# Kernel optimization log

Hardware: AMD Instinct MI355X
Metric: run time of the kernel (lower is better)

The kernel has to match this reference:

```python
import jax, jax.numpy as jnp
import numpy as np

B, S, H = 2, 2048, 4096
NH = 32
HD = H // NH  # 128


def setup_inputs() -> dict:
    key = jax.random.key(0)
    ks = jax.random.split(key, 8)
    scale = 0.02
    hidden_states = jax.random.normal(ks[0], (B, S, H), jnp.float32)
    residual = jax.random.normal(ks[1], (B, S, H), jnp.float32)
    # ALiBi bias per (batch*head) over kv positions, broadcast over q dim
    alibi = jax.random.normal(ks[2], (B * NH, 1, S), jnp.float32) * 0.1
    # causal mask: True where attention is disallowed (j > i)
    causal = jnp.triu(jnp.ones((S, S), dtype=bool), k=1)
    attention_mask = jnp.broadcast_to(causal[None, None], (B, 1, S, S))
    W_qkv = jax.random.normal(ks[3], (3 * H, H), jnp.float32) * scale
    b_qkv = jax.random.normal(ks[4], (3 * H,), jnp.float32) * scale
    W_dense = jax.random.normal(ks[5], (H, H), jnp.float32) * scale
    b_dense = jax.random.normal(ks[6], (H,), jnp.float32) * scale
    return {
        "hidden_states": hidden_states,
        "residual": residual,
        "alibi": alibi,
        "attention_mask": attention_mask,
        "W_qkv": W_qkv,
        "b_qkv": b_qkv,
        "W_dense": W_dense,
        "b_dense": b_dense,
    }


def reference(hidden_states, residual, alibi, attention_mask, W_qkv, b_qkv, W_dense, b_dense):
    b, s, h = hidden_states.shape
    inv_norm = 1.0 / np.sqrt(HD).astype(np.float32)
    # fused QKV projection: [B,S,3H]
    fused = jnp.einsum("bsh,oh->bso", hidden_states, W_qkv) + b_qkv
    fused = fused.reshape(b, s, NH, 3, HD)
    q, k, v = fused[..., 0, :], fused[..., 1, :], fused[..., 2, :]  # [B,S,NH,HD]
    # scores = alibi + inv_norm * Q K^T   (baddbmm with beta=1, alpha=inv_norm)
    scores = jnp.einsum("bqhd,bkhd->bhqk", q, k) * inv_norm
    scores = scores + alibi.reshape(b, NH, 1, s)
    attn_weights = jnp.where(attention_mask, jnp.float32(-100000.0), scores)
    probs = jax.nn.softmax(attn_weights.astype(jnp.float32), axis=-1).astype(scores.dtype)
    # context: [B,S,NH,HD] -> merge heads -> [B,S,H]
    ctx = jnp.einsum("bhqk,bkhd->bqhd", probs, v).reshape(b, s, h)
    out = jnp.einsum("bsh,oh->bso", ctx, W_dense) + b_dense
    return residual + out
```

## Files before the change

### kernel.cpp

```cpp
#include <hip/hip_runtime.h>

#define B_ 2
#define S_ 2048
#define H_ 4096
#define NH_ 32
#define HD_ 128
#define LOG2E 1.44269504088896340736f

typedef unsigned short u16;
typedef __bf16 bf16x8 __attribute__((ext_vector_type(8)));
typedef float floatx4 __attribute__((ext_vector_type(4)));

__device__ __forceinline__ u16 f2bf(float f) {
  union { float f; unsigned u; } v;
  v.f = f;
  unsigned r = v.u + 0x7FFFu + ((v.u >> 16) & 1u);
  return (u16)(r >> 16);
}

__device__ __forceinline__ void dma16(const u16* g, u16* l) {
  __builtin_amdgcn_global_load_lds(
      (const __attribute__((address_space(1))) void*)g,
      (__attribute__((address_space(3))) void*)l, 16, 0, 0);
}

__global__ __launch_bounds__(256) void cast_f32_bf16(const float* __restrict__ in,
                                                     u16* __restrict__ out, int n4) {
  int i = blockIdx.x * 256 + threadIdx.x;
  if (i >= n4) return;
  float4 f = reinterpret_cast<const float4*>(in)[i];
  ushort4 o;
  o.x = f2bf(f.x); o.y = f2bf(f.y); o.z = f2bf(f.z); o.w = f2bf(f.w);
  reinterpret_cast<ushort4*>(out)[i] = o;
}

template<int EPI>
__global__ __launch_bounds__(256) void gemm_bt(
    const u16* __restrict__ A, const u16* __restrict__ Bm, int K,
    const float* __restrict__ bias, const float* __restrict__ resid,
    float* __restrict__ outf,
    u16* __restrict__ qo, u16* __restrict__ ko, u16* __restrict__ vto) {
  __shared__ __align__(16) u16 sA[128 * 32];
  __shared__ __align__(16) u16 sB[128 * 32];
  const int tid  = threadIdx.x;
  const int wave = tid >> 6, lane = tid & 63;
  const int lrow = lane & 15, quad = lane >> 4;
  const int wm = (wave >> 1) * 64, wn = (wave & 1) * 64;
  const int m0 = blockIdx.y * 128, n0 = blockIdx.x * 128;

  const u16* gA[2]; const u16* gB[2];
#pragma unroll
  for (int jj = 0; jj < 2; ++jj) {
    int L  = wave * 16 + jj * 8 + (lane >> 3);
    int sp = (lane & 7) ^ (L & 7);
    int row = 2 * L + (sp >> 2), kc = (sp & 3) * 8;
    gA[jj] = A + (size_t)(m0 + row) * K + kc;
    gB[jj] = Bm + (size_t)(n0 + row) * K + kc;
  }

  const int ssw  = (((lrow & 1) << 2) | quad) ^ ((lrow >> 1) & 7);
  const int aoff = ((wm + lrow) >> 1) * 64 + ssw * 8;
  const int boff = ((wn + lrow) >> 1) * 64 + ssw * 8;

  const floatx4 zf = {0.f, 0.f, 0.f, 0.f};
  floatx4 acc[4][4];
#pragma unroll
  for (int i = 0; i < 4; ++i)
#pragma unroll
    for (int j = 0; j < 4; ++j) acc[i][j] = zf;

  for (int k0 = 0; k0 < K; k0 += 32) {
    __syncthreads();
#pragma unroll
    for (int jj = 0; jj < 2; ++jj) {
      dma16(gA[jj], &sA[(wave * 2 + jj) * 512]);
      dma16(gB[jj], &sB[(wave * 2 + jj) * 512]);
      gA[jj] += 32; gB[jj] += 32;
    }
    __syncthreads();

    bf16x8 af[4], bf[4];
#pragma unroll
    for (int mi = 0; mi < 4; ++mi) af[mi] = *(const bf16x8*)&sA[aoff + mi * 512];
#pragma unroll
    for (int ni = 0; ni < 4; ++ni) bf[ni] = *(const bf16x8*)&sB[boff + ni * 512];
#pragma unroll
    for (int mi = 0; mi < 4; ++mi)
#pragma unroll
      for (int ni = 0; ni < 4; ++ni)
        acc[mi][ni] = __builtin_amdgcn_mfma_f32_16x16x32_bf16(af[mi], bf[ni], acc[mi][ni], 0, 0, 0);
  }

#pragma unroll
  for (int mi = 0; mi < 4; ++mi)
#pragma unroll
    for (int ni = 0; ni < 4; ++ni)
#pragma unroll
      for (int r = 0; r < 4; ++r) {
        int m = m0 + wm + mi * 16 + quad * 4 + r;
        int n = n0 + wn + ni * 16 + lrow;
        float v = acc[mi][ni][r] + bias[n];
        if (EPI == 0) {
          int b = m >> 11, s = m & (S_ - 1);
          int nh = n / (3 * HD_);
          int rem = n - nh * 3 * HD_;
          int which = rem >> 7, d = rem & (HD_ - 1);
          int bh = b * NH_ + nh;
          if (which == 0)      qo[(bh * S_ + s) * HD_ + d] = f2bf(v * 0.08838834764831845f);
          else if (which == 1) ko[(bh * S_ + s) * HD_ + d] = f2bf(v);
          else                 vto[(bh * HD_ + d) * S_ + s] = f2bf(v);
        } else {
          int idx = m * H_ + n;
          outf[idx] = v + resid[idx];
        }
      }
}

#define SKSTR 136
#define SVSTR 72
#define SPSTR 72

__global__ __launch_bounds__(256) void attn_kernel(
    const u16* __restrict__ Qb, const u16* __restrict__ Kb,
    const u16* __restrict__ Vt, const float* __restrict__ alibi,
    u16* __restrict__ ctx) {
  __shared__ __align__(16) u16 sK[64 * SKSTR];
  __shared__ __align__(16) u16 sV[128 * SVSTR];
  __shared__ __align__(16) u16 sP[4 * 16 * SPSTR];
  const int tid  = threadIdx.x;
  const int wave = tid >> 6, lane = tid & 63;
  const int lrow = lane & 15, quad = lane >> 4;
  const int qt = blockIdx.x, bh = blockIdx.y;
  const int qbase = qt * 64;
  const int qrow0 = qbase + wave * 16 + quad * 4;

  const floatx4 zf = {0.f, 0.f, 0.f, 0.f};

  bf16x8 aq[4];
  {
    const u16* qptr = Qb + (bh * S_ + qbase + wave * 16 + lrow) * HD_;
#pragma unroll
    for (int kc = 0; kc < 4; ++kc) aq[kc] = *(const bf16x8*)(qptr + kc * 32 + quad * 8);
  }

  floatx4 o[8];
#pragma unroll
  for (int di = 0; di < 8; ++di) o[di] = zf;
  float m_r[4] = {-1e30f, -1e30f, -1e30f, -1e30f};
  float l_r[4] = {0.f, 0.f, 0.f, 0.f};
  u16* sp = &sP[wave * 16 * SPSTR];

  for (int t = 0; t <= qt; ++t) {
    const int kv0 = t * 64;
    __syncthreads();
#pragma unroll
    for (int rr = 0; rr < 4; ++rr) {
      int flat = rr * 256 + tid;
      {
        int row = flat >> 4, c = flat & 15;
        *(uint4*)&sK[row * SKSTR + c * 8] =
            *(const uint4*)&Kb[(bh * S_ + kv0 + row) * HD_ + c * 8];
      }
      {
        int row = flat >> 3, c = flat & 7;
        *(uint4*)&sV[row * SVSTR + c * 8] =
            *(const uint4*)&Vt[(bh * HD_ + row) * S_ + kv0 + c * 8];
      }
    }
    __syncthreads();

    floatx4 sc[4];
#pragma unroll
    for (int ni = 0; ni < 4; ++ni) {
      floatx4 a = zf;
#pragma unroll
      for (int kc = 0; kc < 4; ++kc) {
        bf16x8 bfrag = *(const bf16x8*)&sK[(ni * 16 + lrow) * SKSTR + kc * 32 + quad * 8];
        a = __builtin_amdgcn_mfma_f32_16x16x32_bf16(aq[kc], bfrag, a, 0, 0, 0);
      }
      sc[ni] = a;
    }

    float al[4];
#pragma unroll
    for (int ni = 0; ni < 4; ++ni) al[ni] = alibi[bh * S_ + kv0 + ni * 16 + lrow];
    const bool diag = (t == qt);

    float p[4][4], alpha[4];
#pragma unroll
    for (int r = 0; r < 4; ++r) {
      float mx = -1e30f;
#pragma unroll
      for (int ni = 0; ni < 4; ++ni) {
        float scv = sc[ni][r] + al[ni];
        if (diag && (kv0 + ni * 16 + lrow) > (qrow0 + r)) scv = -1e30f;
        p[ni][r] = scv;
        mx = fmaxf(mx, scv);
      }
#pragma unroll
      for (int off = 1; off < 16; off <<= 1) mx = fmaxf(mx, __shfl_xor(mx, off));
      float mn = fmaxf(m_r[r], mx);
      float a_ = exp2f((m_r[r] - mn) * LOG2E);
      float s_ = 0.f;
#pragma unroll
      for (int ni = 0; ni < 4; ++ni) {
        float pv = exp2f((p[ni][r] - mn) * LOG2E);
        p[ni][r] = pv;
        s_ += pv;
      }
#pragma unroll
      for (int off = 1; off < 16; off <<= 1) s_ += __shfl_xor(s_, off);
      l_r[r] = l_r[r] * a_ + s_;
      m_r[r] = mn;
      alpha[r] = a_;
    }
#pragma unroll
    for (int di = 0; di < 8; ++di)
#pragma unroll
      for (int r = 0; r < 4; ++r) o[di][r] *= alpha[r];

#pragma unroll
    for (int ni = 0; ni < 4; ++ni)
#pragma unroll
      for (int r = 0; r < 4; ++r)
        sp[(quad * 4 + r) * SPSTR + ni * 16 + lrow] = f2bf(p[ni][r]);
    __syncthreads();

#pragma unroll
    for (int kc = 0; kc < 2; ++kc) {
      bf16x8 afrag = *(const bf16x8*)&sp[lrow * SPSTR + kc * 32 + quad * 8];
#pragma unroll
      for (int di = 0; di < 8; ++di) {
        bf16x8 bfrag = *(const bf16x8*)&sV[(di * 16 + lrow) * SVSTR + kc * 32 + quad * 8];
        o[di] = __builtin_amdgcn_mfma_f32_16x16x32_bf16(afrag, bfrag, o[di], 0, 0, 0);
      }
    }
  }

  const int b = bh >> 5, nh = bh & (NH_ - 1);
#pragma unroll
  for (int di = 0; di < 8; ++di)
#pragma unroll
    for (int r = 0; r < 4; ++r) {
      int q = qrow0 + r;
      float v = o[di][r] / l_r[r];
      ctx[(b * S_ + q) * H_ + nh * HD_ + di * 16 + lrow] = f2bf(v);
    }
}

extern "C" void kernel_launch(void* const* d_in, const int* in_sizes, int n_in,
                              void* d_out, int out_size, void* d_ws, size_t ws_size,
                              hipStream_t stream) {
  const float* hs    = (const float*)d_in[0];
  const float* resid = (const float*)d_in[1];
  const float* alibi = (const float*)d_in[2];
  const float* Wqkv  = (const float*)d_in[4];
  const float* bqkv  = (const float*)d_in[5];
  const float* Wd    = (const float*)d_in[6];
  const float* bd    = (const float*)d_in[7];
  float* out = (float*)d_out;

  u16* ws = (u16*)d_ws;
  u16* hs_bf  = ws;
  u16* ctx_bf = ws;
  u16* w_bf   = ws + 16777216;
  u16* Qb     = ws + 67108864;
  u16* Kb     = ws + 83886080;
  u16* Vtb    = ws + 100663296;

  cast_f32_bf16<<<16384, 256, 0, stream>>>(hs, hs_bf, 4194304);
  cast_f32_bf16<<<49152, 256, 0, stream>>>(Wqkv, w_bf, 12582912);
  gemm_bt<0><<<dim3(96, 32), 256, 0, stream>>>(hs_bf, w_bf, 4096, bqkv,
                                               nullptr, nullptr, Qb, Kb, Vtb);
  attn_kernel<<<dim3(32, 64), 256, 0, stream>>>(Qb, Kb, Vtb, alibi, ctx_bf);
  cast_f32_bf16<<<16384, 256, 0, stream>>>(Wd, w_bf, 4194304);
  gemm_bt<1><<<dim3(32, 32), 256, 0, stream>>>(ctx_bf, w_bf, 4096, bd,
                                               resid, out, nullptr, nullptr, nullptr);
}
```

Baseline: 1.608 ms.

## Rewrite GEMM as 256x256 tiled, double-buffered pipeline with XCD block swizzle

Replaces the 128x128, single-buffered GEMM (barrier per 32-wide K step) with a 256x256 tile run by 512 threads (8 waves). It uses double-buffered 64-wide K stages loaded by global_load_lds DMA, and interleaves the loads with MFMA groups under explicit barriers, waitcnt and setprio. A block-id remap groups workgroups by chiplet to improve L2 reuse. The cost being attacked is exposed memory latency and low arithmetic intensity in both projection GEMMs. In exchange it uses larger LDS and register footprints, and its fragile manual vmcnt accounting relies on K being a power of two (masked prefetch past the end).

New measurement: 1.352 ms. 1.19x faster.

```diff
diff --git a/kernel.cpp b/kernel.cpp
--- a/kernel.cpp
+++ b/kernel.cpp
@@ -34,72 +34,160 @@
   reinterpret_cast<ushort4*>(out)[i] = o;
 }
 
-template<int EPI>
-__global__ __launch_bounds__(256) void gemm_bt(
+#define MM(d, a_, b_) d = __builtin_amdgcn_mfma_f32_16x16x32_bf16(a_, b_, d, 0, 0, 0)
+#define BARX() do { __builtin_amdgcn_s_barrier(); __builtin_amdgcn_sched_barrier(0); } while (0)
+#define LGK0() do { asm volatile("s_waitcnt lgkmcnt(0)" ::: "memory"); __builtin_amdgcn_sched_barrier(0); } while (0)
+#define VMC6() do { asm volatile("s_waitcnt vmcnt(6)" ::: "memory"); } while (0)
+#define PRIO1() __builtin_amdgcn_s_setprio(1)
+#define PRIO0() __builtin_amdgcn_s_setprio(0)
+
+#define STGA(b, h, kk)                                                      \
+  do {                                                                      \
+    const u16* _g = pA + ((h) ? rh : (size_t)0) + (size_t)((kk) & kmsk);    \
+    dma16(_g, &sA[b][h][wave * 512]);                                       \
+    dma16(_g + ro1, &sA[b][h][4096 + wave * 512]);                          \
+  } while (0)
+#define STGB(b, h, kk)                                                      \
+  do {                                                                      \
+    const u16* _g = pB + ((h) ? rh : (size_t)0) + (size_t)((kk) & kmsk);    \
+    dma16(_g, &sB[b][h][wave * 512]);                                       \
+    dma16(_g + ro1, &sB[b][h][4096 + wave * 512]);                          \
+  } while (0)
+
+#define HALF(b, ST1, ST2, ST3, ST4)                                         \
+  {                                                                         \
+    const char* baA = (const char*)&sA[b][wm][0];                           \
+    const char* baB = (const char*)&sB[b][wn >> 1][(wn & 1) * 4096];        \
+    bf16x8 x00 = *(const bf16x8*)(baA + 0 * 2048 + fo0);                    \
+    bf16x8 x01 = *(const bf16x8*)(baA + 0 * 2048 + fo1);                    \
+    bf16x8 x10 = *(const bf16x8*)(baA + 1 * 2048 + fo0);                    \
+    bf16x8 x11 = *(const bf16x8*)(baA + 1 * 2048 + fo1);                    \
+    bf16x8 q00 = *(const bf16x8*)(baB + 0 * 2048 + fo0);                    \
+    bf16x8 q01 = *(const bf16x8*)(baB + 0 * 2048 + fo1);                    \
+    bf16x8 q10 = *(const bf16x8*)(baB + 1 * 2048 + fo0);                    \
+    bf16x8 q11 = *(const bf16x8*)(baB + 1 * 2048 + fo1);                    \
+    bf16x8 q20 = *(const bf16x8*)(baB + 2 * 2048 + fo0);                    \
+    bf16x8 q21 = *(const bf16x8*)(baB + 2 * 2048 + fo1);                    \
+    bf16x8 q30 = *(const bf16x8*)(baB + 3 * 2048 + fo0);                    \
+    bf16x8 q31 = *(const bf16x8*)(baB + 3 * 2048 + fo1);                    \
+    ST1;                                                                    \
+    BARX(); LGK0(); PRIO1();                                                \
+    MM(acc[0][0], x00, q00); MM(acc[0][0], x01, q01);                       \
+    MM(acc[0][1], x00, q10); MM(acc[0][1], x01, q11);                       \
+    MM(acc[0][2], x00, q20); MM(acc[0][2], x01, q21);                       \
+    MM(acc[0][3], x00, q30); MM(acc[0][3], x01, q31);                       \
+    MM(acc[1][0], x10, q00); MM(acc[1][0], x11, q01);                       \
+    MM(acc[1][1], x10, q10); MM(acc[1][1], x11, q11);                       \
+    MM(acc[1][2], x10, q20); MM(acc[1][2], x11, q21);                       \
+    MM(acc[1][3], x10, q30); MM(acc[1][3], x11, q31);                       \
+    PRIO0(); BARX();                                                        \
+    bf16x8 y00 = *(const bf16x8*)(baA + 2 * 2048 + fo0);                    \
+    bf16x8 y01 = *(const bf16x8*)(baA + 2 * 2048 + fo1);                    \
+    bf16x8 y10 = *(const bf16x8*)(baA + 3 * 2048 + fo0);                    \
+    bf16x8 y11 = *(const bf16x8*)(baA + 3 * 2048 + fo1);                    \
+    ST2;                                                                    \
+    BARX(); LGK0(); PRIO1();                                                \
+    MM(acc[2][0], y00, q00); MM(acc[2][0], y01, q01);                       \
+    MM(acc[2][1], y00, q10); MM(acc[2][1], y01, q11);                       \
+    MM(acc[2][2], y00, q20); MM(acc[2][2], y01, q21);                       \
+    MM(acc[2][3], y00, q30); MM(acc[2][3], y01, q31);                       \
+    MM(acc[3][0], y10, q00); MM(acc[3][0], y11, q01);                       \
+    MM(acc[3][1], y10, q10); MM(acc[3][1], y11, q11);                       \
+    MM(acc[3][2], y10, q20); MM(acc[3][2], y11, q21);                       \
+    MM(acc[3][3], y10, q30); MM(acc[3][3], y11, q31);                       \
+    PRIO0(); BARX();                                                        \
+    bf16x8 z00 = *(const bf16x8*)(baA + 4 * 2048 + fo0);                    \
+    bf16x8 z01 = *(const bf16x8*)(baA + 4 * 2048 + fo1);                    \
+    bf16x8 z10 = *(const bf16x8*)(baA + 5 * 2048 + fo0);                    \
+    bf16x8 z11 = *(const bf16x8*)(baA + 5 * 2048 + fo1);                    \
+    bf16x8 w00 = *(const bf16x8*)(baA + 6 * 2048 + fo0);                    \
+    bf16x8 w01 = *(const bf16x8*)(baA + 6 * 2048 + fo1);                    \
+    bf16x8 w10 = *(const bf16x8*)(baA + 7 * 2048 + fo0);                    \
+    bf16x8 w11 = *(const bf16x8*)(baA + 7 * 2048 + fo1);                    \
+    ST3;                                                                    \
+    BARX(); LGK0(); PRIO1();                                                \
+    MM(acc[4][0], z00, q00); MM(acc[4][0], z01, q01);                       \
+    MM(acc[4][1], z00, q10); MM(acc[4][1], z01, q11);                       \
+    MM(acc[4][2], z00, q20); MM(acc[4][2], z01, q21);                       \
+    MM(acc[4][3], z00, q30); MM(acc[4][3], z01, q31);                       \
+    MM(acc[5][0], z10, q00); MM(acc[5][0], z11, q01);                       \
+    MM(acc[5][1], z10, q10); MM(acc[5][1], z11, q11);                       \
+    MM(acc[5][2], z10, q20); MM(acc[5][2], z11, q21);                       \
+    MM(acc[5][3], z10, q30); MM(acc[5][3], z11, q31);                       \
+    PRIO0(); BARX();                                                        \
+    ST4;                                                                    \
+    VMC6(); BARX(); PRIO1();                                                \
+    MM(acc[6][0], w00, q00); MM(acc[6][0], w01, q01);                       \
+    MM(acc[6][1], w00, q10); MM(acc[6][1], w01, q11);                       \
+    MM(acc[6][2], w00, q20); MM(acc[6][2], w01, q21);                       \
+    MM(acc[6][3], w00, q30); MM(acc[6][3], w01, q31);                       \
+    MM(acc[7][0], w10, q00); MM(acc[7][0], w11, q01);                       \
+    MM(acc[7][1], w10, q10); MM(acc[7][1], w11, q11);                       \
+    MM(acc[7][2], w10, q20); MM(acc[7][2], w11, q21);                       \
+    MM(acc[7][3], w10, q30); MM(acc[7][3], w11, q31);                       \
+    PRIO0(); BARX();                                                        \
+  }
+
+template <int EPI>
+__global__ __launch_bounds__(512, 2) void gemm_bt(
     const u16* __restrict__ A, const u16* __restrict__ Bm, int K,
     const float* __restrict__ bias, const float* __restrict__ resid,
     float* __restrict__ outf,
     u16* __restrict__ qo, u16* __restrict__ ko, u16* __restrict__ vto) {
-  __shared__ __align__(16) u16 sA[128 * 32];
-  __shared__ __align__(16) u16 sB[128 * 32];
-  const int tid  = threadIdx.x;
+  __shared__ __align__(16) u16 sA[2][2][8192];
+  __shared__ __align__(16) u16 sB[2][2][8192];
+  const int tid = threadIdx.x;
   const int wave = tid >> 6, lane = tid & 63;
   const int lrow = lane & 15, quad = lane >> 4;
-  const int wm = (wave >> 1) * 64, wn = (wave & 1) * 64;
-  const int m0 = blockIdx.y * 128, n0 = blockIdx.x * 128;
-
-  const u16* gA[2]; const u16* gB[2];
-#pragma unroll
-  for (int jj = 0; jj < 2; ++jj) {
-    int L  = wave * 16 + jj * 8 + (lane >> 3);
-    int sp = (lane & 7) ^ (L & 7);
-    int row = 2 * L + (sp >> 2), kc = (sp & 3) * 8;
-    gA[jj] = A + (size_t)(m0 + row) * K + kc;
-    gB[jj] = Bm + (size_t)(n0 + row) * K + kc;
+  const int wm = wave >> 2, wn = wave & 3;
+  const int kmsk = K - 1;
+
+  int bid = blockIdx.y * gridDim.x + blockIdx.x;
+  const int nwg = gridDim.x * gridDim.y;
+  bid = (bid & 7) * (nwg >> 3) + (bid >> 3);
+  const int bx = bid % gridDim.x, by = bid / gridDim.x;
+  const int m0 = by * 256, n0 = bx * 256;
+
+  const int rthr = tid >> 3;
+  const int cthr = ((tid & 7) ^ (rthr & 7)) * 8;
+  const u16* pA = A + (size_t)(m0 + rthr) * K + cthr;
+  const u16* pB = Bm + (size_t)(n0 + rthr) * K + cthr;
+  const size_t ro1 = (size_t)64 * K;
+  const size_t rh = (size_t)128 * K;
+
+  const int fo0 = lrow * 128 + ((quad ^ (lrow & 7)) << 4);
+  const int fo1 = lrow * 128 + (((4 + quad) ^ (lrow & 7)) << 4);
+
+  const floatx4 zf = {0.f, 0.f, 0.f, 0.f};
+  floatx4 acc[8][4];
+#pragma unroll
+  for (int i = 0; i < 8; ++i)
+#pragma unroll
+    for (int j = 0; j < 4; ++j) acc[i][j] = zf;
+
+  STGB(0, 0, 0); STGB(0, 1, 0); STGA(0, 0, 0); STGA(0, 1, 0);
+  STGB(1, 0, 64); STGB(1, 1, 64); STGA(1, 0, 64);
+  VMC6(); BARX();
+
+  const int NIT = K >> 7;
+#pragma unroll 1
+  for (int it = 0; it < NIT; ++it) {
+    const int kt1 = it * 128 + 64;
+    const int kt2 = it * 128 + 128;
+    const int kt3 = it * 128 + 192;
+    HALF(0, STGA(1, 1, kt1), STGB(0, 0, kt2), STGB(0, 1, kt2), STGA(0, 0, kt2))
+    HALF(1, STGA(0, 1, kt2), STGB(1, 0, kt3), STGB(1, 1, kt3), STGA(1, 0, kt3))
   }
 
-  const int ssw  = (((lrow & 1) << 2) | quad) ^ ((lrow >> 1) & 7);
-  const int aoff = ((wm + lrow) >> 1) * 64 + ssw * 8;
-  const int boff = ((wn + lrow) >> 1) * 64 + ssw * 8;
-
-  const floatx4 zf = {0.f, 0.f, 0.f, 0.f};
-  floatx4 acc[4][4];
-#pragma unroll
-  for (int i = 0; i < 4; ++i)
-#pragma unroll
-    for (int j = 0; j < 4; ++j) acc[i][j] = zf;
-
-  for (int k0 = 0; k0 < K; k0 += 32) {
-    __syncthreads();
-#pragma unroll
-    for (int jj = 0; jj < 2; ++jj) {
-      dma16(gA[jj], &sA[(wave * 2 + jj) * 512]);
-      dma16(gB[jj], &sB[(wave * 2 + jj) * 512]);
-      gA[jj] += 32; gB[jj] += 32;
-    }
-    __syncthreads();
-
-    bf16x8 af[4], bf[4];
-#pragma unroll
-    for (int mi = 0; mi < 4; ++mi) af[mi] = *(const bf16x8*)&sA[aoff + mi * 512];
-#pragma unroll
-    for (int ni = 0; ni < 4; ++ni) bf[ni] = *(const bf16x8*)&sB[boff + ni * 512];
-#pragma unroll
-    for (int mi = 0; mi < 4; ++mi)
-#pragma unroll
-      for (int ni = 0; ni < 4; ++ni)
-        acc[mi][ni] = __builtin_amdgcn_mfma_f32_16x16x32_bf16(af[mi], bf[ni], acc[mi][ni], 0, 0, 0);
-  }
-
-#pragma unroll
-  for (int mi = 0; mi < 4; ++mi)
-#pragma unroll
-    for (int ni = 0; ni < 4; ++ni)
+#pragma unroll
+  for (int f = 0; f < 8; ++f)
+#pragma unroll
+    for (int g = 0; g < 4; ++g)
 #pragma unroll
       for (int r = 0; r < 4; ++r) {
-        int m = m0 + wm + mi * 16 + quad * 4 + r;
-        int n = n0 + wn + ni * 16 + lrow;
-        float v = acc[mi][ni][r] + bias[n];
+        int m = m0 + wm * 128 + f * 16 + quad * 4 + r;
+        int n = n0 + wn * 64 + g * 16 + lrow;
+        float v = acc[f][g][r] + bias[n];
         if (EPI == 0) {
           int b = m >> 11, s = m & (S_ - 1);
           int nh = n / (3 * HD_);
@@ -270,10 +358,10 @@
 
   cast_f32_bf16<<<16384, 256, 0, stream>>>(hs, hs_bf, 4194304);
   cast_f32_bf16<<<49152, 256, 0, stream>>>(Wqkv, w_bf, 12582912);
-  gemm_bt<0><<<dim3(96, 32), 256, 0, stream>>>(hs_bf, w_bf, 4096, bqkv,
+  gemm_bt<0><<<dim3(48, 16), 512, 0, stream>>>(hs_bf, w_bf, 4096, bqkv,
                                                nullptr, nullptr, Qb, Kb, Vtb);
   attn_kernel<<<dim3(32, 64), 256, 0, stream>>>(Qb, Kb, Vtb, alibi, ctx_bf);
   cast_f32_bf16<<<16384, 256, 0, stream>>>(Wd, w_bf, 4194304);
-  gemm_bt<1><<<dim3(32, 32), 256, 0, stream>>>(ctx_bf, w_bf, 4096, bd,
+  gemm_bt<1><<<dim3(16, 16), 512, 0, stream>>>(ctx_bf, w_bf, 4096, bd,
                                                resid, out, nullptr, nullptr, nullptr);
 }
```
